# Performance work log

Hardware: AMD Instinct MI355X
Metric: run time of the kernel (lower is better)

The kernel has to match this reference:

```python
import jax, jax.numpy as jnp
import numpy as np

B, C, T = 64, 384, 512
DUR_MAX = 8            # durations drawn from [0, 8)
MAX_NEW_TIME = 4096    # static padded output length >= T * (DUR_MAX - 1)


def setup_inputs() -> dict:
    key = jax.random.key(0)
    kx, kd = jax.random.split(key)
    x = jax.random.normal(kx, (B, C, T), dtype=jnp.float32)
    duration = jax.random.randint(kd, (B, 1, T), 0, DUR_MAX, dtype=jnp.int32)
    return {"x": x, "duration": duration}


def reference(x, duration):
    # x: [B, C, T] float32, duration: [B, 1, T] int32
    dur = duration[:, 0, :]                      # [B, T]
    csum = jnp.cumsum(dur, axis=-1)              # [B, T] exclusive-right cumsum boundaries
    total = csum[:, -1]                          # [B] expanded length per sample
    j = jnp.arange(MAX_NEW_TIME, dtype=jnp.int32)  # output frame positions
    # source phoneme index for each output frame: smallest t with j < csum[t]
    idx = jax.vmap(lambda c: jnp.searchsorted(c, j, side="right"))(csum)  # [B, MAX_NEW_TIME]
    idx = jnp.clip(idx, 0, T - 1)
    # gather along time, broadcast over channels -> [B, C, MAX_NEW_TIME]
    out = jnp.take_along_axis(x, idx[:, None, :].astype(jnp.int32), axis=-1)
    valid = j[None, :] < total[:, None]          # [B, MAX_NEW_TIME]
    out = jnp.where(valid[:, None, :], out, jnp.zeros((), dtype=x.dtype))
    # mask derived from non-zero values of channel 0, matching torch code
    new_mask = (out[:, 0:1, :] != 0).astype(jnp.int32)  # [B, 1, MAX_NEW_TIME]
    return out, new_mask
```

## Files before the change

kernel.cpp:

```cpp
#include <hip/hip_runtime.h>


#define BB 64
#define CC 384
#define TT 512
#define TOUT 4096
#define CB 16

__global__ __launch_bounds__(TT) void build_idx_kernel(
    const int* __restrict__ dur, int* __restrict__ idx) {
  const int b = blockIdx.x;
  const int t = threadIdx.x;

  __shared__ int s[TT];
  const int d = dur[b * TT + t];
  s[t] = d;
  __syncthreads();

  for (int off = 1; off < TT; off <<= 1) {
    int v = (t >= off) ? s[t - off] : 0;
    __syncthreads();
    s[t] += v;
    __syncthreads();
  }

  const int end = s[t];
  const int start = end - d;

  int* __restrict__ idxb = idx + b * TOUT;
  #pragma unroll
  for (int k = 0; k < TOUT / TT; ++k) idxb[t + k * TT] = -1;
  __syncthreads();

  for (int p = start; p < end; ++p) idxb[p] = t;
}

__global__ __launch_bounds__(256) void gather_kernel(
    const float* __restrict__ x, const int* __restrict__ idx,
    float* __restrict__ out, float* __restrict__ mask) {
  const int b = blockIdx.y;
  const int c0 = blockIdx.x * CB;
  const int tid = threadIdx.x;

  __shared__ float xs[CB * TT];

  const float4* __restrict__ xb4 =
      (const float4*)(x + ((size_t)b * CC + c0) * TT);
  float4* __restrict__ xs4 = (float4*)xs;
  #pragma unroll
  for (int k = 0; k < (CB * TT / 4) / 256; ++k)
    xs4[k * 256 + tid] = xb4[k * 256 + tid];

  const int4* __restrict__ ib4 = (const int4*)(idx + (size_t)b * TOUT);
  int4 I[TOUT / 1024];
  #pragma unroll
  for (int jt = 0; jt < TOUT / 1024; ++jt)
    I[jt] = ib4[jt * 256 + tid];

  __syncthreads();

  float* __restrict__ ob = out + ((size_t)b * CC + c0) * TOUT + tid * 4;

  #pragma unroll
  for (int c = 0; c < CB; ++c) {
    const float* __restrict__ xr = xs + c * TT;
    #pragma unroll
    for (int jt = 0; jt < TOUT / 1024; ++jt) {
      const int4 i4 = I[jt];
      float4 v;
      v.x = (i4.x >= 0) ? xr[i4.x] : 0.0f;
      v.y = (i4.y >= 0) ? xr[i4.y] : 0.0f;
      v.z = (i4.z >= 0) ? xr[i4.z] : 0.0f;
      v.w = (i4.w >= 0) ? xr[i4.w] : 0.0f;
      *(float4*)(ob + (size_t)c * TOUT + jt * 1024) = v;

      if (c == 0 && c0 == 0) {
        float4 m;
        m.x = (v.x != 0.0f) ? 1.0f : 0.0f;
        m.y = (v.y != 0.0f) ? 1.0f : 0.0f;
        m.z = (v.z != 0.0f) ? 1.0f : 0.0f;
        m.w = (v.w != 0.0f) ? 1.0f : 0.0f;
        *(float4*)(mask + (size_t)b * TOUT + jt * 1024 + tid * 4) = m;
      }
    }
  }
}

extern "C" void kernel_launch(void* const* d_in, const int* in_sizes, int n_in,
                              void* d_out, int out_size, void* d_ws, size_t ws_size,
                              hipStream_t stream) {
  const float* x = (const float*)d_in[0];
  const int* dur = (const int*)d_in[1];

  float* out = (float*)d_out;
  float* mask = out + (size_t)BB * CC * TOUT;

  int* idx = (int*)d_ws;

  build_idx_kernel<<<BB, TT, 0, stream>>>(dur, idx);
  gather_kernel<<<dim3(CC / CB, BB), 256, 0, stream>>>(x, idx, out, mask);
}
```

Baseline: 431.8 us.

## Pad shared rows with a zero sentinel and loop two channel tiles per block

```diff
diff --git a/kernel.cpp b/kernel.cpp
--- a/kernel.cpp
+++ b/kernel.cpp
@@ -6,6 +6,9 @@
 #define TT 512
 #define TOUT 4096
 #define CB 16
+#define ROW4 129
+#define ROWF (ROW4*4)
+#define TILES_PER_BLK 2
 
 __global__ __launch_bounds__(TT) void build_idx_kernel(
     const int* __restrict__ dur, int* __restrict__ idx) {
@@ -29,7 +32,7 @@
 
   int* __restrict__ idxb = idx + b * TOUT;
   #pragma unroll
-  for (int k = 0; k < TOUT / TT; ++k) idxb[t + k * TT] = -1;
+  for (int k = 0; k < TOUT / TT; ++k) idxb[t + k * TT] = TT;
   __syncthreads();
 
   for (int p = start; p < end; ++p) idxb[p] = t;
@@ -39,17 +42,9 @@
     const float* __restrict__ x, const int* __restrict__ idx,
     float* __restrict__ out, float* __restrict__ mask) {
   const int b = blockIdx.y;
-  const int c0 = blockIdx.x * CB;
   const int tid = threadIdx.x;
 
-  __shared__ float xs[CB * TT];
-
-  const float4* __restrict__ xb4 =
-      (const float4*)(x + ((size_t)b * CC + c0) * TT);
-  float4* __restrict__ xs4 = (float4*)xs;
-  #pragma unroll
-  for (int k = 0; k < (CB * TT / 4) / 256; ++k)
-    xs4[k * 256 + tid] = xb4[k * 256 + tid];
+  __shared__ float xs[CB * ROWF];
 
   const int4* __restrict__ ib4 = (const int4*)(idx + (size_t)b * TOUT);
   int4 I[TOUT / 1024];
@@ -57,32 +52,50 @@
   for (int jt = 0; jt < TOUT / 1024; ++jt)
     I[jt] = ib4[jt * 256 + tid];
 
-  __syncthreads();
-
-  float* __restrict__ ob = out + ((size_t)b * CC + c0) * TOUT + tid * 4;
+  float4* __restrict__ xs4 = (float4*)xs;
 
   #pragma unroll
-  for (int c = 0; c < CB; ++c) {
-    const float* __restrict__ xr = xs + c * TT;
+  for (int s = 0; s < TILES_PER_BLK; ++s) {
+    const int c0 = (blockIdx.x * TILES_PER_BLK + s) * CB;
+
+    const float4* __restrict__ xb4 =
+        (const float4*)(x + ((size_t)b * CC + c0) * TT);
     #pragma unroll
-    for (int jt = 0; jt < TOUT / 1024; ++jt) {
-      const int4 i4 = I[jt];
-      float4 v;
-      v.x = (i4.x >= 0) ? xr[i4.x] : 0.0f;
-      v.y = (i4.y >= 0) ? xr[i4.y] : 0.0f;
-      v.z = (i4.z >= 0) ? xr[i4.z] : 0.0f;
-      v.w = (i4.w >= 0) ? xr[i4.w] : 0.0f;
-      *(float4*)(ob + (size_t)c * TOUT + jt * 1024) = v;
+    for (int k = 0; k < (CB * TT / 4) / 256; ++k) {
+      const int k2 = k * 256 + tid;
+      const int row = k2 >> 7;
+      const int col = k2 & 127;
+      xs4[row * ROW4 + col] = xb4[k2];
+    }
+    if (tid < CB) xs4[tid * ROW4 + 128] = make_float4(0.f, 0.f, 0.f, 0.f);
+    __syncthreads();
 
-      if (c == 0 && c0 == 0) {
-        float4 m;
-        m.x = (v.x != 0.0f) ? 1.0f : 0.0f;
-        m.y = (v.y != 0.0f) ? 1.0f : 0.0f;
-        m.z = (v.z != 0.0f) ? 1.0f : 0.0f;
-        m.w = (v.w != 0.0f) ? 1.0f : 0.0f;
-        *(float4*)(mask + (size_t)b * TOUT + jt * 1024 + tid * 4) = m;
+    float* __restrict__ ob = out + ((size_t)b * CC + c0) * TOUT + tid * 4;
+
+    #pragma unroll
+    for (int c = 0; c < CB; ++c) {
+      const float* __restrict__ xr = xs + c * ROWF;
+      #pragma unroll
+      for (int jt = 0; jt < TOUT / 1024; ++jt) {
+        const int4 i4 = I[jt];
+        float4 v;
+        v.x = xr[i4.x];
+        v.y = xr[i4.y];
+        v.z = xr[i4.z];
+        v.w = xr[i4.w];
+        *(float4*)(ob + (size_t)c * TOUT + jt * 1024) = v;
+
+        if (c == 0 && c0 == 0) {
+          float4 m;
+          m.x = (v.x != 0.0f) ? 1.0f : 0.0f;
+          m.y = (v.y != 0.0f) ? 1.0f : 0.0f;
+          m.z = (v.z != 0.0f) ? 1.0f : 0.0f;
+          m.w = (v.w != 0.0f) ? 1.0f : 0.0f;
+          *(float4*)(mask + (size_t)b * TOUT + jt * 1024 + tid * 4) = m;
+        }
       }
     }
+    __syncthreads();
   }
 }
 
@@ -98,5 +111,6 @@
   int* idx = (int*)d_ws;
 
   build_idx_kernel<<<BB, TT, 0, stream>>>(dur, idx);
-  gather_kernel<<<dim3(CC / CB, BB), 256, 0, stream>>>(x, idx, out, mask);
+  gather_kernel<<<dim3(CC / CB / TILES_PER_BLK, BB), 256, 0, stream>>>(
+      x, idx, out, mask);
 }
```

New measurement: 457.3 us. 5.9% more time.
